# Kernel optimization log

Measured on AMD Instinct MI355X. Metric: run time of the kernel, lower is better.

Reference implementation:

```python
import jax, jax.numpy as jnp
import numpy as np
import math

B, S, IN = 16, 512, 8
D, H, L, FF, OUT = 512, 8, 4, 2048, 1
VAR_DIM = D // IN  # 64, even -> only sin/cos even-dim path in the original loop
HD = D // H
EPS = 1e-5


def setup_inputs() -> dict:
    key = jax.random.key(0)
    ks = jax.random.split(key, 20)
    s = 0.02
    inp = {
        "features": jax.random.normal(ks[0], (B, S, IN), dtype=jnp.float32),
        "position_indices": jax.random.randint(ks[1], (B, S), 0, 512, dtype=jnp.int64 if jax.config.jax_enable_x64 else jnp.int32),
        "w_in": jax.random.normal(ks[2], (IN, D), dtype=jnp.float32) * s,
        "b_in": jnp.zeros((D,), jnp.float32),
        "qkv_w": jax.random.normal(ks[3], (L, D, 3 * D), dtype=jnp.float32) * s,
        "qkv_b": jnp.zeros((L, 3 * D), jnp.float32),
        "attn_out_w": jax.random.normal(ks[4], (L, D, D), dtype=jnp.float32) * s,
        "attn_out_b": jnp.zeros((L, D), jnp.float32),
        "ln1_g": jnp.ones((L, D), jnp.float32),
        "ln1_b": jnp.zeros((L, D), jnp.float32),
        "ff1_w": jax.random.normal(ks[5], (L, D, FF), dtype=jnp.float32) * s,
        "ff1_b": jnp.zeros((L, FF), jnp.float32),
        "ff2_w": jax.random.normal(ks[6], (L, FF, D), dtype=jnp.float32) * s,
        "ff2_b": jnp.zeros((L, D), jnp.float32),
        "ln2_g": jnp.ones((L, D), jnp.float32),
        "ln2_b": jnp.zeros((L, D), jnp.float32),
        "w_out": jax.random.normal(ks[7], (D, OUT), dtype=jnp.float32) * s,
        "b_out": jnp.zeros((OUT,), jnp.float32),
    }
    return inp


def _pos_encoding(position_indices):
    # Vectorized replacement of the per-(b,i) Python loop.
    pos = position_indices.astype(jnp.float32)  # [B,S]
    div = jnp.exp(jnp.arange(0, VAR_DIM, 2, dtype=jnp.float32) * (-(math.log(10000.0) / VAR_DIM)))  # [VAR_DIM//2]
    ang = pos[:, :, None] * div  # [B,S,VAR_DIM//2]
    # interleave sin (even dims) / cos (odd dims) -> [B,S,VAR_DIM]
    block = jnp.stack([jnp.sin(ang), jnp.cos(ang)], axis=-1).reshape(pos.shape[0], pos.shape[1], VAR_DIM)
    # identical encoding per variable since var_positions == position_indices for all vars
    return jnp.tile(block, (1, 1, IN))  # [B,S,D]


def _layer_norm(x, g, b):
    mu = jnp.mean(x, axis=-1, keepdims=True)
    var = jnp.mean(jnp.square(x - mu), axis=-1, keepdims=True)
    return (x - mu) * jax.lax.rsqrt(var + EPS) * g + b


def _encoder_layer(x, qkv_w, qkv_b, ow, ob, g1, b1, f1w, f1b, f2w, f2b, g2, b2):
    Bx, Sx, _ = x.shape
    qkv = x @ qkv_w + qkv_b  # [B,S,3D]
    q, k, v = jnp.split(qkv, 3, axis=-1)
    q = q.reshape(Bx, Sx, H, HD)
    k = k.reshape(Bx, Sx, H, HD)
    v = v.reshape(Bx, Sx, H, HD)
    scores = jnp.einsum("bqhd,bkhd->bhqk", q, k) / math.sqrt(HD)
    attn = jax.nn.softmax(scores, axis=-1)
    ctx = jnp.einsum("bhqk,bkhd->bqhd", attn, v).reshape(Bx, Sx, D)
    attn_out = ctx @ ow + ob
    x = _layer_norm(x + attn_out, g1, b1)  # post-norm (PyTorch default norm_first=False)
    ff = jax.nn.relu(x @ f1w + f1b) @ f2w + f2b
    return _layer_norm(x + ff, g2, b2)


def reference(features, position_indices, w_in, b_in, qkv_w, qkv_b, attn_out_w, attn_out_b,
              ln1_g, ln1_b, ff1_w, ff1_b, ff2_w, ff2_b, ln2_g, ln2_b, w_out, b_out):
    x = features @ w_in + b_in  # input projection
    x = x + _pos_encoding(position_indices)
    for l in range(L):
        x = _encoder_layer(x, qkv_w[l], qkv_b[l], attn_out_w[l], attn_out_b[l],
                           ln1_g[l], ln1_b[l], ff1_w[l], ff1_b[l], ff2_w[l], ff2_b[l],
                           ln2_g[l], ln2_b[l])
    return x @ w_out + b_out  # [B,S,OUT]
```

## Files before the change

### kernel.cpp

```cpp
#include <hip/hip_runtime.h>
#include <cstdint>
#include <cstddef>

#define BATCH   16
#define SEQ     512
#define NTOK    8192
#define DMODEL  512
#define NHEAD   8
#define HDIM    64
#define FFDIM   2048
#define NLAYER  4

typedef unsigned short u16;
typedef __attribute__((ext_vector_type(8))) short bf16x8;
typedef __attribute__((ext_vector_type(8))) unsigned short us8;
typedef __attribute__((ext_vector_type(4))) float f32x4;

__device__ __forceinline__ float bf2f(u16 u) {
    union { float f; unsigned int i; } x; x.i = ((unsigned int)u) << 16; return x.f;
}
__device__ __forceinline__ u16 f2b(float f) {
    union { float f; unsigned int u; } a; a.f = f;
    unsigned int r = a.u + 0x7fff + ((a.u >> 16) & 1);
    return (u16)(r >> 16);
}

__device__ __forceinline__ void async_copy16(const void* g, void* l) {
    __builtin_amdgcn_global_load_lds(
        (const __attribute__((address_space(1))) unsigned int*)g,
        (__attribute__((address_space(3))) unsigned int*)l, 16, 0, 0);
}

__global__ __launch_bounds__(256) void embed_kernel(
    const float* __restrict__ feat, const int* __restrict__ pos,
    const float* __restrict__ w_in, const float* __restrict__ b_in,
    u16* __restrict__ xb)
{
    int idx = blockIdx.x * 256 + threadIdx.x;
    if (idx >= NTOK * DMODEL) return;
    int t = idx >> 9;
    int d = idx & 511;
    float acc = b_in[d];
#pragma unroll
    for (int i = 0; i < 8; ++i)
        acc += feat[t * 8 + i] * w_in[i * DMODEL + d];
    int p = pos[t];
    int dl = d & 63;
    int pair = dl >> 1;
    float div = expf(-(float)(2 * pair) * 0.14391156831212787f);
    float ang = (float)p * div;
    float pe = (dl & 1) ? cosf(ang) : sinf(ang);
    xb[idx] = f2b(acc + pe);
}

__global__ __launch_bounds__(256) void transpose_w_kernel(
    const float* __restrict__ W, u16* __restrict__ WT, int K, int N)
{
    __shared__ float t[32][33];
    const float* Wl = W + (size_t)blockIdx.z * K * N;
    u16* WTl = WT + (size_t)blockIdx.z * K * N;
    int n0 = blockIdx.x * 32, k0 = blockIdx.y * 32;
    int c = threadIdx.x & 31, r8 = threadIdx.x >> 5;
#pragma unroll
    for (int i = 0; i < 4; ++i) {
        int r = r8 + i * 8;
        t[r][c] = Wl[(size_t)(k0 + r) * N + n0 + c];
    }
    __syncthreads();
#pragma unroll
    for (int i = 0; i < 4; ++i) {
        int r = r8 + i * 8;
        WTl[(size_t)(n0 + r) * K + k0 + c] = f2b(t[c][r]);
    }
}

template <int RELU, int ADD_RESID>
__global__ __launch_bounds__(256) void gemm_bk64_kernel(
    const u16* __restrict__ A, const u16* __restrict__ BT,
    const float* __restrict__ bias, const u16* __restrict__ resid,
    u16* __restrict__ C, int M, int N, int K)
{
    __shared__ u16 As[128 * 64];
    __shared__ u16 Bs[128 * 64];
    const int tid = threadIdx.x;

    const int gx = gridDim.x, gy = gridDim.y;
    const int raw = blockIdx.x + gx * blockIdx.y;
    const int xcd = raw & 7;
    const int k8  = raw >> 3;
    const int ych = gy >> 3;
    const int m0 = (xcd * ych + k8 / gx) * 128;
    const int n0 = (k8 % gx) * 128;

    const int wid = tid >> 6, lane = tid & 63;
    const int wr = (wid >> 1) * 64, wc = (wid & 1) * 64;
    const int lr = lane & 15, lk16 = lane >> 4;
    const int sw = lr & 7;

    f32x4 acc[4][4] = {};

    for (int kt = 0; kt < K; kt += 64) {
        __syncthreads();
#pragma unroll
        for (int u = 0; u < 4; ++u) {
            int cc = u * 256 + tid;
            int row = cc >> 3, kc = cc & 7;
            async_copy16(&A[(size_t)(m0 + row) * K + kt + ((kc ^ (row & 7)) * 8)],
                         &As[cc * 8]);
        }
#pragma unroll
        for (int u = 0; u < 4; ++u) {
            int cc = u * 256 + tid;
            int row = cc >> 3, kc = cc & 7;
            async_copy16(&BT[(size_t)(n0 + row) * K + kt + ((kc ^ (row & 7)) * 8)],
                         &Bs[cc * 8]);
        }
        __syncthreads();

        bf16x8 a[4][2], b[4][2];
#pragma unroll
        for (int i = 0; i < 4; ++i)
#pragma unroll
            for (int kk = 0; kk < 2; ++kk) {
                a[i][kk] = *(const bf16x8*)&As[
                    (wr + i * 16 + lr) * 64 + (((kk * 4 + lk16) ^ sw) * 8)];
                b[i][kk] = *(const bf16x8*)&Bs[
                    (wc + i * 16 + lr) * 64 + (((kk * 4 + lk16) ^ sw) * 8)];
            }

        __builtin_amdgcn_s_setprio(1);
#pragma unroll
        for (int i = 0; i < 4; ++i)
#pragma unroll
            for (int j = 0; j < 4; ++j)
#pragma unroll
                for (int kk = 0; kk < 2; ++kk)
                    acc[i][j] = __builtin_amdgcn_mfma_f32_16x16x32_bf16(
                        a[i][kk], b[j][kk], acc[i][j], 0, 0, 0);
        __builtin_amdgcn_s_setprio(0);
    }

#pragma unroll
    for (int j = 0; j < 4; ++j) {
        int col = n0 + wc + j * 16 + lr;
        float bb = bias[col];
#pragma unroll
        for (int i = 0; i < 4; ++i) {
            int rbase = m0 + wr + i * 16 + lk16 * 4;
            f32x4 v = acc[i][j];
#pragma unroll
            for (int r = 0; r < 4; ++r) {
                float val = v[r] + bb;
                if (ADD_RESID) val += bf2f(resid[(size_t)(rbase + r) * N + col]);
                if (RELU) val = fmaxf(val, 0.f);
                C[(size_t)(rbase + r) * N + col] = f2b(val);
            }
        }
    }
}

__global__ __launch_bounds__(256) void attention_mfma_kernel(
    const u16* __restrict__ qkv, u16* __restrict__ ctx)
{
    __shared__ __align__(16) u16 Ks[2][64 * 64];
    __shared__ __align__(16) u16 Vt[64][72];
    __shared__ __align__(16) u16 Ps[4][16][72];

    const int tid = threadIdx.x;
    const int raw = blockIdx.x;
    const int xcd = raw & 7;
    const int k8  = raw >> 3;
    const int bh  = xcd * 16 + (k8 >> 3);
    const int b = bh >> 3, h = bh & 7;
    const int q0 = (k8 & 7) * 64;

    const int wid = tid >> 6, lane = tid & 63;
    const int lr = lane & 15;
    const int lk16 = lane >> 4;
    const size_t base = (size_t)b * SEQ * 1536;
    const int qrow = wid * 16 + lr;

    bf16x8 qf[2];
#pragma unroll
    for (int ks = 0; ks < 2; ++ks)
        qf[ks] = *(const bf16x8*)&qkv[base + (size_t)(q0 + qrow) * 1536 + h * 64
                                      + ks * 32 + lk16 * 8];

    const int vr0 = tid & 63;
    const int vc0 = (tid >> 6) * 8;
    const int vc1 = 32 + vc0;

#pragma unroll
    for (int j = 0; j < 2; ++j) {
        int c = j * 256 + tid;
        int row = c >> 3;
        int sc8 = ((c & 7) ^ (row & 7)) * 8;
        async_copy16(&qkv[base + (size_t)(row) * 1536 + 512 + h * 64 + sc8], &Ks[0][c * 8]);
    }
    us8 v0 = *(const us8*)&qkv[base + (size_t)(vr0) * 1536 + 1024 + h * 64 + vc0];
    us8 v1 = *(const us8*)&qkv[base + (size_t)(vr0) * 1536 + 1024 + h * 64 + vc1];
    __syncthreads();
#pragma unroll
    for (int e = 0; e < 8; ++e) { Vt[vc0 + e][vr0] = v0[e]; Vt[vc1 + e][vr0] = v1[e]; }
    __syncthreads();

    float l_r[4] = {0.f, 0.f, 0.f, 0.f};
    f32x4 o_acc[4] = {};
    const float SC2 = 0.18033688011112042f;

    for (int t = 0; t < SEQ / 64; ++t) {
        const int cur = t & 1;
        const bool more = (t + 1 < SEQ / 64);
        if (more) {
            const int kt1 = (t + 1) * 64;
#pragma unroll
            for (int j = 0; j < 2; ++j) {
                int c = j * 256 + tid;
                int row = c >> 3;
                int sc8 = ((c & 7) ^ (row & 7)) * 8;
                async_copy16(&qkv[base + (size_t)(kt1 + row) * 1536 + 512 + h * 64 + sc8],
                             &Ks[cur ^ 1][c * 8]);
            }
            v0 = *(const us8*)&qkv[base + (size_t)(kt1 + vr0) * 1536 + 1024 + h * 64 + vc0];
            v1 = *(const us8*)&qkv[base + (size_t)(kt1 + vr0) * 1536 + 1024 + h * 64 + vc1];
        }

        f32x4 sc[4] = {};
#pragma unroll
        for (int ks = 0; ks < 2; ++ks) {
#pragma unroll
            for (int j = 0; j < 4; ++j) {
                int krow = j * 16 + lr;
                bf16x8 bk = *(const bf16x8*)&Ks[cur][krow * 64 + ((ks * 4 + lk16) ^ (krow & 7)) * 8];
                sc[j] = __builtin_amdgcn_mfma_f32_16x16x32_bf16(qf[ks], bk, sc[j], 0, 0, 0);
            }
        }

        float pf[4][4];
#pragma unroll
        for (int r = 0; r < 4; ++r) {
            float s0 = 0.f;
#pragma unroll
            for (int j = 0; j < 4; ++j) {
                float p = __builtin_amdgcn_exp2f(sc[j][r] * SC2);
                pf[j][r] = p;
                s0 += p;
            }
#pragma unroll
            for (int m = 1; m < 16; m <<= 1)
                s0 += __shfl_xor(s0, m);
            l_r[r] += s0;
        }

#pragma unroll
        for (int j = 0; j < 4; ++j)
#pragma unroll
            for (int r = 0; r < 4; ++r)
                Ps[wid][lk16 * 4 + r][j * 16 + lr] = f2b(pf[j][r]);

#pragma unroll
        for (int kk = 0; kk < 2; ++kk) {
            bf16x8 ap = *(const bf16x8*)&Ps[wid][lr][kk * 32 + lk16 * 8];
#pragma unroll
            for (int j2 = 0; j2 < 4; ++j2) {
                bf16x8 bv = *(const bf16x8*)&Vt[j2 * 16 + lr][kk * 32 + lk16 * 8];
                o_acc[j2] = __builtin_amdgcn_mfma_f32_16x16x32_bf16(ap, bv, o_acc[j2], 0, 0, 0);
            }
        }

        __syncthreads();
        if (more) {
#pragma unroll
            for (int e = 0; e < 8; ++e) { Vt[vc0 + e][vr0] = v0[e]; Vt[vc1 + e][vr0] = v1[e]; }
        }
        __syncthreads();
    }

#pragma unroll
    for (int r = 0; r < 4; ++r) {
        float inv = 1.f / l_r[r];
        int t = b * SEQ + q0 + wid * 16 + lk16 * 4 + r;
        u16* op = &ctx[(size_t)t * DMODEL + h * 64];
#pragma unroll
        for (int j2 = 0; j2 < 4; ++j2)
            op[j2 * 16 + lr] = f2b(o_acc[j2][r] * inv);
    }
}

__global__ __launch_bounds__(256) void ln_kernel(
    const u16* __restrict__ sum_in, u16* __restrict__ xb,
    const float* __restrict__ gamma, const float* __restrict__ beta)
{
    const int wave = threadIdx.x >> 6, lane = threadIdx.x & 63;
    const int t = blockIdx.x * 4 + wave;
    const u16* sr = sum_in + (size_t)t * DMODEL;
    u16* xbr = xb + (size_t)t * DMODEL;

    us8 a = *(const us8*)&sr[lane * 8];
    float v[8];
    float sum = 0.f;
#pragma unroll
    for (int i = 0; i < 8; ++i) { v[i] = bf2f(a[i]); sum += v[i]; }
#pragma unroll
    for (int off = 32; off; off >>= 1) sum += __shfl_xor(sum, off);
    float mean = sum * (1.f / DMODEL);
    float vs = 0.f;
#pragma unroll
    for (int i = 0; i < 8; ++i) {
        float d = v[i] - mean;
        vs += d * d;
    }
#pragma unroll
    for (int off = 32; off; off >>= 1) vs += __shfl_xor(vs, off);
    float rstd = rsqrtf(vs * (1.f / DMODEL) + 1e-5f);
    us8 o;
#pragma unroll
    for (int i = 0; i < 8; ++i) {
        int d = lane * 8 + i;
        o[i] = f2b((v[i] - mean) * rstd * gamma[d] + beta[d]);
    }
    *(us8*)xbr[lane * 8 == 0 ? 0 : 0];
    *(us8*)&xbr[lane * 8] = o;
}

__global__ __launch_bounds__(256) void out_kernel(
    const u16* __restrict__ xb, const float* __restrict__ w,
    const float* __restrict__ b, float* __restrict__ out)
{
    const int wave = threadIdx.x >> 6, lane = threadIdx.x & 63;
    const int t = blockIdx.x * 4 + wave;
    const u16* xr = xb + (size_t)t * DMODEL;
    us8 a = *(const us8*)&xr[lane * 8];
    float acc = 0.f;
#pragma unroll
    for (int i = 0; i < 8; ++i)
        acc += bf2f(a[i]) * w[lane * 8 + i];
#pragma unroll
    for (int off = 32; off; off >>= 1) acc += __shfl_xor(acc, off);
    if (lane == 0) out[t] = acc + b[0];
}

extern "C" void kernel_launch(void* const* d_in, const int* in_sizes, int n_in,
                              void* d_out, int out_size, void* d_ws, size_t ws_size,
                              hipStream_t stream)
{
    const float* features = (const float*)d_in[0];
    const int*   pos      = (const int*)  d_in[1];
    const float* w_in     = (const float*)d_in[2];
    const float* b_in     = (const float*)d_in[3];
    const float* qkv_w    = (const float*)d_in[4];
    const float* qkv_b    = (const float*)d_in[5];
    const float* ow       = (const float*)d_in[6];
    const float* ob       = (const float*)d_in[7];
    const float* g1       = (const float*)d_in[8];
    const float* b1       = (const float*)d_in[9];
    const float* ff1w     = (const float*)d_in[10];
    const float* ff1b     = (const float*)d_in[11];
    const float* ff2w     = (const float*)d_in[12];
    const float* ff2b     = (const float*)d_in[13];
    const float* g2       = (const float*)d_in[14];
    const float* b2       = (const float*)d_in[15];
    const float* w_out    = (const float*)d_in[16];
    const float* b_out    = (const float*)d_in[17];
    float* out = (float*)d_out;

    char* p = (char*)d_ws;
    auto alloc = [&](size_t bytes) { char* r = p; p += (bytes + 255) & ~(size_t)255; return r; };
    u16*   xb  = (u16*)  alloc((size_t)NTOK * DMODEL * 2);
    u16*   big = (u16*)  alloc((size_t)NTOK * FFDIM * 2);
    u16*   ctx = (u16*)  alloc((size_t)NTOK * DMODEL * 2);
    u16*   tmp = (u16*)  alloc((size_t)NTOK * DMODEL * 2);
    u16* wqkvT = (u16*)alloc((size_t)NLAYER * DMODEL * 3 * DMODEL * 2);
    u16* owT   = (u16*)alloc((size_t)NLAYER * DMODEL * DMODEL * 2);
    u16* f1wT  = (u16*)alloc((size_t)NLAYER * DMODEL * FFDIM * 2);
    u16* f2wT  = (u16*)alloc((size_t)NLAYER * FFDIM * DMODEL * 2);

    transpose_w_kernel<<<dim3(3 * DMODEL / 32, DMODEL / 32, NLAYER), 256, 0, stream>>>(
        qkv_w, wqkvT, DMODEL, 3 * DMODEL);
    transpose_w_kernel<<<dim3(DMODEL / 32, DMODEL / 32, NLAYER), 256, 0, stream>>>(
        ow, owT, DMODEL, DMODEL);
    transpose_w_kernel<<<dim3(FFDIM / 32, DMODEL / 32, NLAYER), 256, 0, stream>>>(
        ff1w, f1wT, DMODEL, FFDIM);
    transpose_w_kernel<<<dim3(DMODEL / 32, FFDIM / 32, NLAYER), 256, 0, stream>>>(
        ff2w, f2wT, FFDIM, DMODEL);

    embed_kernel<<<(NTOK * DMODEL + 255) / 256, 256, 0, stream>>>(
        features, pos, w_in, b_in, xb);

    for (int l = 0; l < NLAYER; ++l) {
        gemm_bk64_kernel<0, 0><<<dim3(3 * DMODEL / 128, NTOK / 128), 256, 0, stream>>>(
            xb, wqkvT + (size_t)l * DMODEL * 3 * DMODEL, qkv_b + (size_t)l * 3 * DMODEL,
            nullptr, big, NTOK, 3 * DMODEL, DMODEL);
        attention_mfma_kernel<<<BATCH * NHEAD * (SEQ / 64), 256, 0, stream>>>(big, ctx);
        gemm_bk64_kernel<0, 1><<<dim3(DMODEL / 128, NTOK / 128), 256, 0, stream>>>(
            ctx, owT + (size_t)l * DMODEL * DMODEL, ob + (size_t)l * DMODEL, xb,
            tmp, NTOK, DMODEL, DMODEL);
        ln_kernel<<<NTOK / 4, 256, 0, stream>>>(
            tmp, xb, g1 + (size_t)l * DMODEL, b1 + (size_t)l * DMODEL);
        gemm_bk64_kernel<1, 0><<<dim3(FFDIM / 128, NTOK / 128), 256, 0, stream>>>(
            xb, f1wT + (size_t)l * DMODEL * FFDIM, ff1b + (size_t)l * FFDIM,
            nullptr, big, NTOK, FFDIM, DMODEL);
        gemm_bk64_kernel<0, 1><<<dim3(DMODEL / 128, NTOK / 128), 256, 0, stream>>>(
            big, f2wT + (size_t)l * FFDIM * DMODEL, ff2b + (size_t)l * DMODEL, xb,
            tmp, NTOK, DMODEL, FFDIM);
        ln_kernel<<<NTOK / 4, 256, 0, stream>>>(
            tmp, xb, g2 + (size_t)l * DMODEL, b2 + (size_t)l * DMODEL);
    }

    out_kernel<<<NTOK / 4, 256, 0, stream>>>(xb, w_out, b_out, out);
}
```

Baseline: 598.2 us.

## Overlap GEMM tile loads with MFMA and compute softmax row sums via MFMA

The GEMM main loop now reads each tile's fragments into registers, then issues the async loads for the next K tile before running the MFMAs, so global loads overlap with compute using a single LDS buffer. In attention, the per-row exp sums that used cross-lane shuffles are now computed by an extra MFMA of the bf16 probabilities against a vector of ones, removing the shuffle reductions. This adds one MFMA per kk step and sums the bf16-rounded probabilities, which slightly changes numerics. A stray no-op statement in the layernorm kernel is also removed.

```diff
diff --git a/kernel.cpp b/kernel.cpp
--- a/kernel.cpp
+++ b/kernel.cpp
@@ -98,25 +98,30 @@
     const int sw = lr & 7;
 
     f32x4 acc[4][4] = {};
-
-    for (int kt = 0; kt < K; kt += 64) {
-        __syncthreads();
-#pragma unroll
-        for (int u = 0; u < 4; ++u) {
-            int cc = u * 256 + tid;
-            int row = cc >> 3, kc = cc & 7;
-            async_copy16(&A[(size_t)(m0 + row) * K + kt + ((kc ^ (row & 7)) * 8)],
-                         &As[cc * 8]);
-        }
-#pragma unroll
-        for (int u = 0; u < 4; ++u) {
-            int cc = u * 256 + tid;
-            int row = cc >> 3, kc = cc & 7;
-            async_copy16(&BT[(size_t)(n0 + row) * K + kt + ((kc ^ (row & 7)) * 8)],
-                         &Bs[cc * 8]);
-        }
-        __syncthreads();
-
+    const int T = K >> 6;
+
+#define STAGE_TILE(kt)                                                         \
+    {                                                                          \
+        _Pragma("unroll")                                                      \
+        for (int u = 0; u < 4; ++u) {                                          \
+            int cc = u * 256 + tid;                                            \
+            int row = cc >> 3, kc = cc & 7;                                    \
+            async_copy16(&A[(size_t)(m0 + row) * K + (kt) + ((kc ^ (row & 7)) * 8)], \
+                         &As[cc * 8]);                                         \
+        }                                                                      \
+        _Pragma("unroll")                                                      \
+        for (int u = 0; u < 4; ++u) {                                          \
+            int cc = u * 256 + tid;                                            \
+            int row = cc >> 3, kc = cc & 7;                                    \
+            async_copy16(&BT[(size_t)(n0 + row) * K + (kt) + ((kc ^ (row & 7)) * 8)], \
+                         &Bs[cc * 8]);                                         \
+        }                                                                      \
+    }
+
+    STAGE_TILE(0);
+    __syncthreads();
+
+    for (int t = 0; t < T; ++t) {
         bf16x8 a[4][2], b[4][2];
 #pragma unroll
         for (int i = 0; i < 4; ++i)
@@ -127,6 +132,8 @@
                 b[i][kk] = *(const bf16x8*)&Bs[
                     (wc + i * 16 + lr) * 64 + (((kk * 4 + lk16) ^ sw) * 8)];
             }
+        __syncthreads();
+        if (t + 1 < T) STAGE_TILE((t + 1) * 64);
 
         __builtin_amdgcn_s_setprio(1);
 #pragma unroll
@@ -138,7 +145,10 @@
                     acc[i][j] = __builtin_amdgcn_mfma_f32_16x16x32_bf16(
                         a[i][kk], b[j][kk], acc[i][j], 0, 0, 0);
         __builtin_amdgcn_s_setprio(0);
-    }
+
+        __syncthreads();
+    }
+#undef STAGE_TILE
 
 #pragma unroll
     for (int j = 0; j < 4; ++j) {
@@ -186,6 +196,10 @@
         qf[ks] = *(const bf16x8*)&qkv[base + (size_t)(q0 + qrow) * 1536 + h * 64
                                       + ks * 32 + lk16 * 8];
 
+    bf16x8 ones;
+#pragma unroll
+    for (int e = 0; e < 8; ++e) ones[e] = (short)0x3F80;
+
     const int vr0 = tid & 63;
     const int vc0 = (tid >> 6) * 8;
     const int vc1 = 32 + vc0;
@@ -204,7 +218,7 @@
     for (int e = 0; e < 8; ++e) { Vt[vc0 + e][vr0] = v0[e]; Vt[vc1 + e][vr0] = v1[e]; }
     __syncthreads();
 
-    float l_r[4] = {0.f, 0.f, 0.f, 0.f};
+    f32x4 l_acc = {};
     f32x4 o_acc[4] = {};
     const float SC2 = 0.18033688011112042f;
 
@@ -236,31 +250,17 @@
             }
         }
 
-        float pf[4][4];
-#pragma unroll
-        for (int r = 0; r < 4; ++r) {
-            float s0 = 0.f;
-#pragma unroll
-            for (int j = 0; j < 4; ++j) {
-                float p = __builtin_amdgcn_exp2f(sc[j][r] * SC2);
-                pf[j][r] = p;
-                s0 += p;
-            }
-#pragma unroll
-            for (int m = 1; m < 16; m <<= 1)
-                s0 += __shfl_xor(s0, m);
-            l_r[r] += s0;
-        }
-
 #pragma unroll
         for (int j = 0; j < 4; ++j)
 #pragma unroll
             for (int r = 0; r < 4; ++r)
-                Ps[wid][lk16 * 4 + r][j * 16 + lr] = f2b(pf[j][r]);
+                Ps[wid][lk16 * 4 + r][j * 16 + lr] =
+                    f2b(__builtin_amdgcn_exp2f(sc[j][r] * SC2));
 
 #pragma unroll
         for (int kk = 0; kk < 2; ++kk) {
             bf16x8 ap = *(const bf16x8*)&Ps[wid][lr][kk * 32 + lk16 * 8];
+            l_acc = __builtin_amdgcn_mfma_f32_16x16x32_bf16(ap, ones, l_acc, 0, 0, 0);
 #pragma unroll
             for (int j2 = 0; j2 < 4; ++j2) {
                 bf16x8 bv = *(const bf16x8*)&Vt[j2 * 16 + lr][kk * 32 + lk16 * 8];
@@ -278,7 +278,7 @@
 
 #pragma unroll
     for (int r = 0; r < 4; ++r) {
-        float inv = 1.f / l_r[r];
+        float inv = 1.f / l_acc[r];
         int t = b * SEQ + q0 + wid * 16 + lk16 * 4 + r;
         u16* op = &ctx[(size_t)t * DMODEL + h * 64];
 #pragma unroll
@@ -319,7 +319,6 @@
         int d = lane * 8 + i;
         o[i] = f2b((v[i] - mean) * rstd * gamma[d] + beta[d]);
     }
-    *(us8*)xbr[lane * 8 == 0 ? 0 : 0];
     *(us8*)&xbr[lane * 8] = o;
 }
 
```

Measured after the change: 540.4 us, median of 3. -9.7%, faster.
